# Performance work log

Measured on AMD Instinct MI355X. Metric: run time of the kernel, lower is better.

## Reference

```python
import jax, jax.numpy as jnp
import numpy as np

B, C, H, W = 8, 64, 64, 64
OUT_H, OUT_W = 32, 32


def setup_inputs() -> dict:
    key = jax.random.key(0)
    ks = jax.random.split(key, 9)
    s = 1.0 / np.sqrt(C).astype(np.float32)
    return {
        "x": jax.random.normal(ks[0], (B, C, H, W), jnp.float32),
        "wq": jax.random.normal(ks[1], (C, C), jnp.float32) * s,
        "bq": jax.random.normal(ks[2], (C,), jnp.float32) * 0.01,
        "wk": jax.random.normal(ks[3], (C, C), jnp.float32) * s,
        "bk": jax.random.normal(ks[4], (C,), jnp.float32) * 0.01,
        "wv": jax.random.normal(ks[5], (C, C), jnp.float32) * s,
        "bv": jax.random.normal(ks[6], (C,), jnp.float32) * 0.01,
        "wm": jax.random.normal(ks[7], (C, C), jnp.float32) * s,
        "bm": jax.random.normal(ks[8], (C,), jnp.float32) * 0.01,
    }


def reference(x, wq, bq, wk, bk, wv, bv, wm, bm):
    # pushforward: self-attention over spatial tokens, 1x1-conv mixing + ReLU,
    # then bilinear resize to out_shape (align_corners=False semantics).
    b, c, h, w = x.shape
    t = x.reshape(b, c, h * w).transpose(0, 2, 1)  # [B, HW, C] tokens
    q = jnp.einsum('bnc,dc->bnd', t, wq) + bq      # 1x1 conv == per-pixel linear
    k = jnp.einsum('bnc,dc->bnd', t, wk) + bk
    v = jnp.einsum('bnc,dc->bnd', t, wv) + bv
    scores = jnp.einsum('bnc,bmc->bnm', q, k) / jnp.sqrt(jnp.float32(c))  # [B, HW, HW]
    attn = jax.nn.softmax(scores, axis=-1)
    o = jnp.einsum('bnm,bmc->bnc', attn, v)        # [B, HW, C]
    mixed = jax.nn.relu(jnp.einsum('bnc,dc->bnd', o, wm) + bm)
    out = mixed.transpose(0, 2, 1).reshape(b, c, h, w)
    # F.interpolate(mode='bilinear', align_corners=False) == half-pixel bilinear, no antialias
    out = jax.image.resize(out, (b, c, OUT_H, OUT_W), method='bilinear', antialias=False)
    return out
```

## Files before the change

### kernel.cpp

```cpp
#include <hip/hip_runtime.h>
#include <stdint.h>

typedef unsigned short u16;
typedef unsigned int   u32;
typedef __attribute__((ext_vector_type(8)))  short short8;
typedef __attribute__((ext_vector_type(4)))  float f32x4;
typedef __attribute__((ext_vector_type(16))) float f32x16;

#define NTOK 4096
#define LOG2E 1.44269504088896340736f
#define QS    (0.125f * LOG2E)

__device__ __forceinline__ u16 f2bf(float f) {
    u32 u = __builtin_bit_cast(u32, f);
    u += 0x7fffu + ((u >> 16) & 1u);
    return (u16)(u >> 16);
}
__device__ __forceinline__ float bf2f(u16 v) {
    return __builtin_bit_cast(float, (u32)v << 16);
}
__device__ __forceinline__ u32 pk_hu(float a, float b) {
    u32 ua = __builtin_bit_cast(u32, a) + 0x8000u;
    u32 ub = __builtin_bit_cast(u32, b) + 0x8000u;
    return __builtin_amdgcn_perm(ub, ua, 0x07060302);
}
__device__ __forceinline__ f32x16 zero16() {
    f32x16 v;
#pragma unroll
    for (int i = 0; i < 16; ++i) v[i] = 0.f;
    return v;
}

#define MFMA16x32 __builtin_amdgcn_mfma_f32_16x16x32_bf16
#define MFMA32x16 __builtin_amdgcn_mfma_f32_32x32x16_bf16

__global__ __launch_bounds__(512, 2) void qkv2(
    const float* __restrict__ x,
    const float* __restrict__ wq, const float* __restrict__ bq,
    const float* __restrict__ wk, const float* __restrict__ bk,
    const float* __restrict__ wv, const float* __restrict__ bv,
    u16* __restrict__ Q, u16* __restrict__ K, u16* __restrict__ Vp)
{
    __shared__ __align__(16) u16 Wl[3 * 64 * 72];
    __shared__ __align__(16) u16 Xl[128 * 64];
    const int tid  = threadIdx.x;
    const int b    = blockIdx.x & 7;
    const int sp   = blockIdx.x >> 3;
    const int n0   = sp << 7;
    const int wave = tid >> 6;
    const int lane = tid & 63;
    const int quad = lane >> 4;
    const int l15  = lane & 15;

#pragma unroll
    for (int j = 0; j < 6; ++j) {
        const int idx  = j * 2048 + tid * 4;
        const int mat  = idx >> 12;
        const int ridx = idx & 4095;
        const float* src = (mat == 0) ? wq : (mat == 1) ? wk : wv;
        const float sc = (mat == 0) ? QS : 1.0f;
        const float4 v = *(const float4*)(src + ridx);
        uint2 pk;
        pk.x = (u32)f2bf(v.x * sc) | ((u32)f2bf(v.y * sc) << 16);
        pk.y = (u32)f2bf(v.z * sc) | ((u32)f2bf(v.w * sc) << 16);
        *(uint2*)&Wl[mat * 4608 + (ridx >> 6) * 72 + (ridx & 63)] = pk;
    }

    const int ch = tid >> 3;
    const int tg = tid & 7;
    float4 xs[4];
#pragma unroll
    for (int k = 0; k < 4; ++k)
        xs[k] = *(const float4*)(x + ((size_t)(b * 64 + ch)) * NTOK + n0 + tg * 16 + k * 4);
#pragma unroll
    for (int k = 0; k < 4; ++k) {
        const float vv[4] = {xs[k].x, xs[k].y, xs[k].z, xs[k].w};
#pragma unroll
        for (int e = 0; e < 4; ++e) {
            const int tok = tg * 16 + k * 4 + e;
            Xl[tok * 64 + (((ch >> 3) ^ (tok & 7)) & 7) * 8 + (ch & 7)] = f2bf(vv[e]);
        }
    }
    __syncthreads();

    const int row0 = wave * 16 + l15;
    short8 xf[2];
#pragma unroll
    for (int kk = 0; kk < 2; ++kk)
        xf[kk] = *(const short8*)&Xl[row0 * 64 + (((kk * 4 + quad) ^ (row0 & 7)) & 7) * 8];

    const size_t tokbase = (size_t)b * NTOK + n0 + wave * 16;

#pragma unroll
    for (int mat = 0; mat < 2; ++mat) {
        const float* bias = (mat == 0) ? bq : bk;
        const float bsc = (mat == 0) ? QS : 1.0f;
#pragma unroll
        for (int mt = 0; mt < 4; ++mt) {
            const u16* wr = &Wl[mat * 4608 + (mt * 16 + l15) * 72 + quad * 8];
            const short8 wf0 = *(const short8*)(wr);
            const short8 wf1 = *(const short8*)(wr + 32);
            f32x4 acc = {0.f, 0.f, 0.f, 0.f};
            acc = MFMA16x32(wf0, xf[0], acc, 0, 0, 0);
            acc = MFMA16x32(wf1, xf[1], acc, 0, 0, 0);
            const float4 b4 = *(const float4*)(bias + mt * 16 + quad * 4);
            uint2 pk;
            pk.x = (u32)f2bf(acc[0] + b4.x * bsc) | ((u32)f2bf(acc[1] + b4.y * bsc) << 16);
            pk.y = (u32)f2bf(acc[2] + b4.z * bsc) | ((u32)f2bf(acc[3] + b4.w * bsc) << 16);
            u16* dst = (mat == 0) ? Q : K;
            *(uint2*)(dst + (tokbase + l15) * 64 + mt * 16 + quad * 4) = pk;
        }
    }

    __syncthreads();
    u16* Vl = Xl;
    const int tok = wave * 16 + l15;
    const int th  = tok >> 6;
    const int t64 = tok & 63;
#pragma unroll
    for (int mt = 0; mt < 4; ++mt) {
        const u16* wr = &Wl[2 * 4608 + (mt * 16 + l15) * 72 + quad * 8];
        const short8 wf0 = *(const short8*)(wr);
        const short8 wf1 = *(const short8*)(wr + 32);
        f32x4 acc = {0.f, 0.f, 0.f, 0.f};
        acc = MFMA16x32(wf0, xf[0], acc, 0, 0, 0);
        acc = MFMA16x32(wf1, xf[1], acc, 0, 0, 0);
        const float4 b4 = *(const float4*)(bv + mt * 16 + quad * 4);
        const float o[4] = {acc[0] + b4.x, acc[1] + b4.y, acc[2] + b4.z, acc[3] + b4.w};
#pragma unroll
        for (int r = 0; r < 4; ++r) {
            const int d = mt * 16 + quad * 4 + r;
            Vl[(d * 2 + th) * 64 + (((t64 >> 3) ^ ((d >> 1) & 7)) & 7) * 8 + (t64 & 7)] = f2bf(o[r]);
        }
    }
    __syncthreads();

#pragma unroll
    for (int dd = 0; dd < 4; ++dd) {
        const int id   = dd * 512 + tid;
        const int d2   = id >> 5;
        const int tokc = (id & 31) * 4;
        const int thc  = tokc >> 6;
        const int t64c = tokc & 63;
        const int slot = ((t64c >> 3) ^ ((d2 >> 1) & 7)) & 7;
        const uint2 v2 = *(const uint2*)&Vl[(d2 * 2 + thc) * 64 + slot * 8 + (t64c & 7)];
        const int gt = sp * 4 + (tokc >> 5);
        const int tl = tokc & 31;
        const int sl = (tl & 0x13) | (((tl >> 2) & 1) << 3) | (((tl >> 3) & 1) << 2);
        *(uint2*)(Vp + (((size_t)b * 128 + gt) * 64 + d2) * 32 + sl) = v2;
    }
}

__global__ __launch_bounds__(512, 2) void attn8(
    const u16* __restrict__ Q, const u16* __restrict__ K,
    const u16* __restrict__ Vp,
    const float* __restrict__ wm, const float* __restrict__ bm,
    float* __restrict__ out)
{
    __shared__ __align__(16) char smem[54272];
    const int tid  = threadIdx.x;
    const int wave = tid >> 6;
    const int lane = tid & 63;
    const int c31  = lane & 31;
    const int hw   = lane >> 5;
    const int quad = lane >> 4;
    const int l15  = lane & 15;
    const int h    = wave >> 2;
    const int s    = wave & 3;
    const int b    = blockIdx.x & 7;
    const int oh   = blockIdx.x >> 3;
    const int n0   = oh * 128;

    short8 qf[2][4];
#pragma unroll
    for (int nt = 0; nt < 2; ++nt)
#pragma unroll
        for (int ks = 0; ks < 4; ++ks)
            qf[nt][ks] = *(const short8*)(Q + ((size_t)(b * NTOK + n0 + h * 64 + nt * 32 + c31)) * 64
                                            + ks * 16 + hw * 8);

    const u16* Kb  = K + ((size_t)b * NTOK + s * 1024) * 64;
    const u16* Vbp = Vp + ((size_t)b * 128 + s * 32) * 2048;

    f32x16 O[2][2];
#pragma unroll
    for (int mt = 0; mt < 2; ++mt)
#pragma unroll
        for (int nt = 0; nt < 2; ++nt) O[mt][nt] = zero16();
    float lpa[2] = {0.f, 0.f};

    auto load_kv = [&](short8 (&kf)[4], short8 (&vf)[4], int t) {
        const int tc = (t < 32) ? t : 31;
        const u16* kt = Kb + (size_t)tc * 2048;
#pragma unroll
        for (int ks = 0; ks < 4; ++ks)
            kf[ks] = *(const short8*)(kt + c31 * 64 + ks * 16 + hw * 8);
        const u16* vt = Vbp + (size_t)tc * 2048;
#pragma unroll
        for (int mk = 0; mk < 4; ++mk)
            vf[mk] = *(const short8*)(vt + ((mk >> 1) * 32 + c31) * 32 + (mk & 1) * 16 + hw * 8);
    };

    auto S_compute = [&](f32x16 (&sv)[2], const short8 (&kf)[4]) {
#pragma unroll
        for (int nt = 0; nt < 2; ++nt) {
            f32x16 a = zero16();
            a = MFMA32x16(kf[0], qf[nt][0], a, 0, 0, 0);
            a = MFMA32x16(kf[1], qf[nt][1], a, 0, 0, 0);
            a = MFMA32x16(kf[2], qf[nt][2], a, 0, 0, 0);
            a = MFMA32x16(kf[3], qf[nt][3], a, 0, 0, 0);
            sv[nt] = a;
        }
    };

    auto tile_tail = [&](const f32x16 (&sv)[2], const short8 (&vf)[4]) {
#pragma unroll
        for (int nt = 0; nt < 2; ++nt) {
            float p[16];
#pragma unroll
            for (int r = 0; r < 16; ++r) p[r] = __builtin_amdgcn_exp2f(sv[nt][r]);
            lpa[nt] += (((p[0] + p[1]) + (p[2] + p[3])) + ((p[4] + p[5]) + (p[6] + p[7])))
                     + (((p[8] + p[9]) + (p[10] + p[11])) + ((p[12] + p[13]) + (p[14] + p[15])));
            uint4 B0, B1;
            B0.x = pk_hu(p[0],  p[1]);  B0.y = pk_hu(p[2],  p[3]);
            B0.z = pk_hu(p[4],  p[5]);  B0.w = pk_hu(p[6],  p[7]);
            B1.x = pk_hu(p[8],  p[9]);  B1.y = pk_hu(p[10], p[11]);
            B1.z = pk_hu(p[12], p[13]); B1.w = pk_hu(p[14], p[15]);
            const short8 pb0 = __builtin_bit_cast(short8, B0);
            const short8 pb1 = __builtin_bit_cast(short8, B1);
            O[0][nt] = MFMA32x16(vf[0], pb0, O[0][nt], 0, 0, 0);
            O[0][nt] = MFMA32x16(vf[1], pb1, O[0][nt], 0, 0, 0);
            O[1][nt] = MFMA32x16(vf[2], pb0, O[1][nt], 0, 0, 0);
            O[1][nt] = MFMA32x16(vf[3], pb1, O[1][nt], 0, 0, 0);
        }
    };

    short8 kfA[4], vfA[4], kfB[4], vfB[4];
    f32x16 svA[2], svB[2];
    load_kv(kfA, vfA, 0);
    load_kv(kfB, vfB, 1);
    S_compute(svA, kfA);

#pragma unroll 1
    for (int tt = 0; tt < 16; ++tt) {
        const int t0 = tt * 2;
        S_compute(svB, kfB);
        tile_tail(svA, vfA);
        load_kv(kfA, vfA, t0 + 2);
        S_compute(svA, kfA);
        tile_tail(svB, vfB);
        load_kv(kfB, vfB, t0 + 3);
    }

#pragma unroll
    for (int nt = 0; nt < 2; ++nt) lpa[nt] += __shfl_xor(lpa[nt], 32);

    float* lpbuf = (float*)(smem + 52224);
    if (hw == 0) {
#pragma unroll
        for (int nt = 0; nt < 2; ++nt)
            lpbuf[(h * 4 + s) * 64 + nt * 32 + c31] = lpa[nt];
    }
    if (s != 0) {
        u16* sec = (u16*)smem + (h * 3 + s - 1) * 4352;
#pragma unroll
        for (int mt = 0; mt < 2; ++mt)
#pragma unroll
            for (int nt = 0; nt < 2; ++nt)
#pragma unroll
                for (int r = 0; r < 16; ++r) {
                    const int ch = mt * 32 + (r & 3) + 8 * (r >> 2) + 4 * hw;
                    sec[(nt * 32 + c31) * 68 + ch] = f2bf(O[mt][nt][r]);
                }
    }
    __syncthreads();

    float rinv[2];
    if (s == 0) {
#pragma unroll
        for (int nt = 0; nt < 2; ++nt) {
            float sum = 0.f;
#pragma unroll
            for (int sx = 0; sx < 4; ++sx)
                sum += lpbuf[(h * 4 + sx) * 64 + nt * 32 + c31];
            rinv[nt] = 1.0f / sum;
        }
#pragma unroll
        for (int sx = 1; sx < 4; ++sx) {
            const u16* sec = (const u16*)smem + (h * 3 + sx - 1) * 4352;
#pragma unroll
            for (int mt = 0; mt < 2; ++mt)
#pragma unroll
                for (int nt = 0; nt < 2; ++nt)
#pragma unroll
                    for (int r = 0; r < 16; ++r) {
                        const int ch = mt * 32 + (r & 3) + 8 * (r >> 2) + 4 * hw;
                        O[mt][nt][r] += bf2f(sec[(nt * 32 + c31) * 68 + ch]);
                    }
        }
    }
    short8 wB[4][2];
    float bb[4];
#pragma unroll
    for (int nt = 0; nt < 4; ++nt) {
        const int d = nt * 16 + l15;
        const float* wr = wm + (size_t)d * 64 + quad * 8;
        const float4 a0 = *(const float4*)(wr);
        const float4 a1 = *(const float4*)(wr + 4);
        const float4 c0 = *(const float4*)(wr + 32);
        const float4 c1 = *(const float4*)(wr + 36);
        ((u32*)&wB[nt][0])[0] = (u32)f2bf(a0.x) | ((u32)f2bf(a0.y) << 16);
        ((u32*)&wB[nt][0])[1] = (u32)f2bf(a0.z) | ((u32)f2bf(a0.w) << 16);
        ((u32*)&wB[nt][0])[2] = (u32)f2bf(a1.x) | ((u32)f2bf(a1.y) << 16);
        ((u32*)&wB[nt][0])[3] = (u32)f2bf(a1.z) | ((u32)f2bf(a1.w) << 16);
        ((u32*)&wB[nt][1])[0] = (u32)f2bf(c0.x) | ((u32)f2bf(c0.y) << 16);
        ((u32*)&wB[nt][1])[1] = (u32)f2bf(c0.z) | ((u32)f2bf(c0.w) << 16);
        ((u32*)&wB[nt][1])[2] = (u32)f2bf(c1.x) | ((u32)f2bf(c1.y) << 16);
        ((u32*)&wB[nt][1])[3] = (u32)f2bf(c1.z) | ((u32)f2bf(c1.w) << 16);
        bb[nt] = bm[d];
    }
    __syncthreads();

    if (s == 0) {
        u16* M0 = (u16*)smem + h * 4096;
#pragma unroll
        for (int mt = 0; mt < 2; ++mt)
#pragma unroll
            for (int nt = 0; nt < 2; ++nt)
#pragma unroll
                for (int r = 0; r < 16; ++r) {
                    const int lr = nt * 32 + c31;
                    const int ch = mt * 32 + (r & 3) + 8 * (r >> 2) + 4 * hw;
                    const float v = O[mt][nt][r] * rinv[nt];
                    M0[lr * 64 + (((ch >> 3) ^ (lr & 7)) & 7) * 8 + (ch & 7)] = f2bf(v);
                }
    }
    __syncthreads();

    const u16* M0r = (const u16*)smem + (wave >> 2) * 4096;
    const int lr = (wave & 3) * 16 + l15;
    const short8 af0 = *(const short8*)&M0r[lr * 64 + ((quad ^ (lr & 7)) & 7) * 8];
    const short8 af1 = *(const short8*)&M0r[lr * 64 + (((4 + quad) ^ (lr & 7)) & 7) * 8];
    float* Mf = (float*)(smem + 16384);
#pragma unroll
    for (int nt = 0; nt < 4; ++nt) {
        f32x4 acc = {0.f, 0.f, 0.f, 0.f};
        acc = MFMA16x32(af0, wB[nt][0], acc, 0, 0, 0);
        acc = MFMA16x32(af1, wB[nt][1], acc, 0, 0, 0);
#pragma unroll
        for (int r = 0; r < 4; ++r) {
            float v = acc[r] + bb[nt];
            v = v > 0.f ? v : 0.f;
            Mf[(wave * 16 + quad * 4 + r) * 68 + nt * 16 + l15] = v;
        }
    }
    __syncthreads();

    const int ow = tid & 31;
    const int cb = (tid >> 5) & 15;
#pragma unroll
    for (int i = 0; i < 4; ++i) {
        const int c = cb + i * 16;
        const float v = 0.25f * (Mf[(2 * ow) * 68 + c] + Mf[(2 * ow + 1) * 68 + c]
                               + Mf[(64 + 2 * ow) * 68 + c] + Mf[(65 + 2 * ow) * 68 + c]);
        out[((size_t)(b * 64 + c) * 32 + oh) * 32 + ow] = v;
    }
}

extern "C" void kernel_launch(void* const* d_in, const int* in_sizes, int n_in,
                              void* d_out, int out_size, void* d_ws, size_t ws_size,
                              hipStream_t stream) {
    (void)in_sizes; (void)n_in; (void)out_size; (void)ws_size;
    const float* x  = (const float*)d_in[0];
    const float* wq = (const float*)d_in[1];
    const float* bq = (const float*)d_in[2];
    const float* wk = (const float*)d_in[3];
    const float* bk = (const float*)d_in[4];
    const float* wv = (const float*)d_in[5];
    const float* bv = (const float*)d_in[6];
    const float* wm = (const float*)d_in[7];
    const float* bm = (const float*)d_in[8];

    u16* Q  = (u16*)d_ws;
    u16* K  = Q + (size_t)8 * NTOK * 64;
    u16* Vp = K + (size_t)8 * NTOK * 64;

    qkv2<<<256, 512, 0, stream>>>(x, wq, bq, wk, bk, wv, bv, Q, K, Vp);
    attn8<<<256, 512, 0, stream>>>(Q, K, Vp, wm, bm, (float*)d_out);
}
```

Baseline: 136.0 us.

## Fuse QKV projection and attention into one kernel with grid-wide barrier

```diff
diff --git a/kernel.cpp b/kernel.cpp
--- a/kernel.cpp
+++ b/kernel.cpp
@@ -34,15 +34,16 @@
 #define MFMA16x32 __builtin_amdgcn_mfma_f32_16x16x32_bf16
 #define MFMA32x16 __builtin_amdgcn_mfma_f32_32x32x16_bf16
 
-__global__ __launch_bounds__(512, 2) void qkv2(
+__global__ __launch_bounds__(512, 2) void fused_qkv_attn(
     const float* __restrict__ x,
     const float* __restrict__ wq, const float* __restrict__ bq,
     const float* __restrict__ wk, const float* __restrict__ bk,
     const float* __restrict__ wv, const float* __restrict__ bv,
-    u16* __restrict__ Q, u16* __restrict__ K, u16* __restrict__ Vp)
+    const float* __restrict__ wm, const float* __restrict__ bm,
+    u16* __restrict__ K, u16* __restrict__ Vp, u32* __restrict__ ctr,
+    float* __restrict__ out)
 {
-    __shared__ __align__(16) u16 Wl[3 * 64 * 72];
-    __shared__ __align__(16) u16 Xl[128 * 64];
+    __shared__ __align__(16) char smem[62464];
     const int tid  = threadIdx.x;
     const int b    = blockIdx.x & 7;
     const int sp   = blockIdx.x >> 3;
@@ -51,6 +52,10 @@
     const int lane = tid & 63;
     const int quad = lane >> 4;
     const int l15  = lane & 15;
+
+    u16* Wl   = (u16*)smem;
+    u16* Xl   = (u16*)(smem + 27648);
+    u16* Qlds = (u16*)(smem + 44032);
 
 #pragma unroll
     for (int j = 0; j < 6; ++j) {
@@ -66,118 +71,127 @@
         *(uint2*)&Wl[mat * 4608 + (ridx >> 6) * 72 + (ridx & 63)] = pk;
     }
 
-    const int ch = tid >> 3;
-    const int tg = tid & 7;
-    float4 xs[4];
-#pragma unroll
-    for (int k = 0; k < 4; ++k)
-        xs[k] = *(const float4*)(x + ((size_t)(b * 64 + ch)) * NTOK + n0 + tg * 16 + k * 4);
-#pragma unroll
-    for (int k = 0; k < 4; ++k) {
-        const float vv[4] = {xs[k].x, xs[k].y, xs[k].z, xs[k].w};
-#pragma unroll
-        for (int e = 0; e < 4; ++e) {
-            const int tok = tg * 16 + k * 4 + e;
-            Xl[tok * 64 + (((ch >> 3) ^ (tok & 7)) & 7) * 8 + (ch & 7)] = f2bf(vv[e]);
-        }
-    }
-    __syncthreads();
-
-    const int row0 = wave * 16 + l15;
-    short8 xf[2];
-#pragma unroll
-    for (int kk = 0; kk < 2; ++kk)
-        xf[kk] = *(const short8*)&Xl[row0 * 64 + (((kk * 4 + quad) ^ (row0 & 7)) & 7) * 8];
-
-    const size_t tokbase = (size_t)b * NTOK + n0 + wave * 16;
-
-#pragma unroll
-    for (int mat = 0; mat < 2; ++mat) {
-        const float* bias = (mat == 0) ? bq : bk;
-        const float bsc = (mat == 0) ? QS : 1.0f;
+    {
+        const int ch = tid >> 3;
+        const int tg = tid & 7;
+        float4 xs[4];
+#pragma unroll
+        for (int k = 0; k < 4; ++k)
+            xs[k] = *(const float4*)(x + ((size_t)(b * 64 + ch)) * NTOK + n0 + tg * 16 + k * 4);
+#pragma unroll
+        for (int k = 0; k < 4; ++k) {
+            const float vv[4] = {xs[k].x, xs[k].y, xs[k].z, xs[k].w};
+#pragma unroll
+            for (int e = 0; e < 4; ++e) {
+                const int tok = tg * 16 + k * 4 + e;
+                Xl[tok * 64 + (((ch >> 3) ^ (tok & 7)) & 7) * 8 + (ch & 7)] = f2bf(vv[e]);
+            }
+        }
+    }
+    __syncthreads();
+
+    {
+        const int row0 = wave * 16 + l15;
+        short8 xf[2];
+#pragma unroll
+        for (int kk = 0; kk < 2; ++kk)
+            xf[kk] = *(const short8*)&Xl[row0 * 64 + (((kk * 4 + quad) ^ (row0 & 7)) & 7) * 8];
+
+#pragma unroll
+        for (int mat = 0; mat < 2; ++mat) {
+            const float* bias = (mat == 0) ? bq : bk;
+            const float bsc = (mat == 0) ? QS : 1.0f;
+#pragma unroll
+            for (int mt = 0; mt < 4; ++mt) {
+                const u16* wr = &Wl[mat * 4608 + (mt * 16 + l15) * 72 + quad * 8];
+                const short8 wf0 = *(const short8*)(wr);
+                const short8 wf1 = *(const short8*)(wr + 32);
+                f32x4 acc = {0.f, 0.f, 0.f, 0.f};
+                acc = MFMA16x32(wf0, xf[0], acc, 0, 0, 0);
+                acc = MFMA16x32(wf1, xf[1], acc, 0, 0, 0);
+                const float4 b4 = *(const float4*)(bias + mt * 16 + quad * 4);
+                const float o[4] = {acc[0] + b4.x * bsc, acc[1] + b4.y * bsc,
+                                    acc[2] + b4.z * bsc, acc[3] + b4.w * bsc};
+                if (mat == 0) {
+                    const int tok = wave * 16 + l15;
+#pragma unroll
+                    for (int r = 0; r < 4; ++r) {
+                        const int d = mt * 16 + quad * 4 + r;
+                        Qlds[tok * 64 + (((d >> 3) ^ (tok & 7)) & 7) * 8 + (d & 7)] = f2bf(o[r]);
+                    }
+                } else {
+                    uint2 pk;
+                    pk.x = (u32)f2bf(o[0]) | ((u32)f2bf(o[1]) << 16);
+                    pk.y = (u32)f2bf(o[2]) | ((u32)f2bf(o[3]) << 16);
+                    *(uint2*)(K + ((size_t)(b * NTOK + n0 + wave * 16 + l15)) * 64
+                                + mt * 16 + quad * 4) = pk;
+                }
+            }
+        }
+
+        __syncthreads();
+        u16* Vl = Xl;
+        const int tok = wave * 16 + l15;
+        const int th  = tok >> 6;
+        const int t64 = tok & 63;
 #pragma unroll
         for (int mt = 0; mt < 4; ++mt) {
-            const u16* wr = &Wl[mat * 4608 + (mt * 16 + l15) * 72 + quad * 8];
+            const u16* wr = &Wl[2 * 4608 + (mt * 16 + l15) * 72 + quad * 8];
             const short8 wf0 = *(const short8*)(wr);
             const short8 wf1 = *(const short8*)(wr + 32);
             f32x4 acc = {0.f, 0.f, 0.f, 0.f};
             acc = MFMA16x32(wf0, xf[0], acc, 0, 0, 0);
             acc = MFMA16x32(wf1, xf[1], acc, 0, 0, 0);
-            const float4 b4 = *(const float4*)(bias + mt * 16 + quad * 4);
-            uint2 pk;
-            pk.x = (u32)f2bf(acc[0] + b4.x * bsc) | ((u32)f2bf(acc[1] + b4.y * bsc) << 16);
-            pk.y = (u32)f2bf(acc[2] + b4.z * bsc) | ((u32)f2bf(acc[3] + b4.w * bsc) << 16);
-            u16* dst = (mat == 0) ? Q : K;
-            *(uint2*)(dst + (tokbase + l15) * 64 + mt * 16 + quad * 4) = pk;
-        }
-    }
-
-    __syncthreads();
-    u16* Vl = Xl;
-    const int tok = wave * 16 + l15;
-    const int th  = tok >> 6;
-    const int t64 = tok & 63;
-#pragma unroll
-    for (int mt = 0; mt < 4; ++mt) {
-        const u16* wr = &Wl[2 * 4608 + (mt * 16 + l15) * 72 + quad * 8];
-        const short8 wf0 = *(const short8*)(wr);
-        const short8 wf1 = *(const short8*)(wr + 32);
-        f32x4 acc = {0.f, 0.f, 0.f, 0.f};
-        acc = MFMA16x32(wf0, xf[0], acc, 0, 0, 0);
-        acc = MFMA16x32(wf1, xf[1], acc, 0, 0, 0);
-        const float4 b4 = *(const float4*)(bv + mt * 16 + quad * 4);
-        const float o[4] = {acc[0] + b4.x, acc[1] + b4.y, acc[2] + b4.z, acc[3] + b4.w};
-#pragma unroll
-        for (int r = 0; r < 4; ++r) {
-            const int d = mt * 16 + quad * 4 + r;
-            Vl[(d * 2 + th) * 64 + (((t64 >> 3) ^ ((d >> 1) & 7)) & 7) * 8 + (t64 & 7)] = f2bf(o[r]);
-        }
-    }
-    __syncthreads();
-
-#pragma unroll
-    for (int dd = 0; dd < 4; ++dd) {
-        const int id   = dd * 512 + tid;
-        const int d2   = id >> 5;
-        const int tokc = (id & 31) * 4;
-        const int thc  = tokc >> 6;
-        const int t64c = tokc & 63;
-        const int slot = ((t64c >> 3) ^ ((d2 >> 1) & 7)) & 7;
-        const uint2 v2 = *(const uint2*)&Vl[(d2 * 2 + thc) * 64 + slot * 8 + (t64c & 7)];
-        const int gt = sp * 4 + (tokc >> 5);
-        const int tl = tokc & 31;
-        const int sl = (tl & 0x13) | (((tl >> 2) & 1) << 3) | (((tl >> 3) & 1) << 2);
-        *(uint2*)(Vp + (((size_t)b * 128 + gt) * 64 + d2) * 32 + sl) = v2;
-    }
-}
-
-__global__ __launch_bounds__(512, 2) void attn8(
-    const u16* __restrict__ Q, const u16* __restrict__ K,
-    const u16* __restrict__ Vp,
-    const float* __restrict__ wm, const float* __restrict__ bm,
-    float* __restrict__ out)
-{
-    __shared__ __align__(16) char smem[54272];
-    const int tid  = threadIdx.x;
-    const int wave = tid >> 6;
-    const int lane = tid & 63;
-    const int c31  = lane & 31;
-    const int hw   = lane >> 5;
-    const int quad = lane >> 4;
-    const int l15  = lane & 15;
-    const int h    = wave >> 2;
-    const int s    = wave & 3;
-    const int b    = blockIdx.x & 7;
-    const int oh   = blockIdx.x >> 3;
-    const int n0   = oh * 128;
+            const float4 b4 = *(const float4*)(bv + mt * 16 + quad * 4);
+            const float o[4] = {acc[0] + b4.x, acc[1] + b4.y, acc[2] + b4.z, acc[3] + b4.w};
+#pragma unroll
+            for (int r = 0; r < 4; ++r) {
+                const int d = mt * 16 + quad * 4 + r;
+                Vl[(d * 2 + th) * 64 + (((t64 >> 3) ^ ((d >> 1) & 7)) & 7) * 8 + (t64 & 7)] = f2bf(o[r]);
+            }
+        }
+        __syncthreads();
+
+#pragma unroll
+        for (int dd = 0; dd < 4; ++dd) {
+            const int id   = dd * 512 + tid;
+            const int d2   = id >> 5;
+            const int tokc = (id & 31) * 4;
+            const int thc  = tokc >> 6;
+            const int t64c = tokc & 63;
+            const int slot = ((t64c >> 3) ^ ((d2 >> 1) & 7)) & 7;
+            const uint2 v2 = *(const uint2*)&Vl[(d2 * 2 + thc) * 64 + slot * 8 + (t64c & 7)];
+            const int gt = sp * 4 + (tokc >> 5);
+            const int tl = tokc & 31;
+            const int sl = (tl & 0x13) | (((tl >> 2) & 1) << 3) | (((tl >> 3) & 1) << 2);
+            *(uint2*)(Vp + (((size_t)b * 128 + gt) * 64 + d2) * 32 + sl) = v2;
+        }
+    }
+
+    __threadfence();
+    __syncthreads();
+    if (tid == 0) {
+        __hip_atomic_fetch_add(ctr, 1u, __ATOMIC_RELEASE, __HIP_MEMORY_SCOPE_AGENT);
+        while (__hip_atomic_load(ctr, __ATOMIC_ACQUIRE, __HIP_MEMORY_SCOPE_AGENT) < 256u)
+            __builtin_amdgcn_s_sleep(8);
+    }
+    __syncthreads();
+    __threadfence();
+
+    const int c31 = lane & 31;
+    const int hw  = lane >> 5;
+    const int h   = wave >> 2;
+    const int s   = wave & 3;
 
     short8 qf[2][4];
 #pragma unroll
     for (int nt = 0; nt < 2; ++nt)
 #pragma unroll
-        for (int ks = 0; ks < 4; ++ks)
-            qf[nt][ks] = *(const short8*)(Q + ((size_t)(b * NTOK + n0 + h * 64 + nt * 32 + c31)) * 64
-                                            + ks * 16 + hw * 8);
+        for (int ks = 0; ks < 4; ++ks) {
+            const int tok = h * 64 + nt * 32 + c31;
+            const int slot = ((ks * 2 + hw) ^ (tok & 7)) & 7;
+            qf[nt][ks] = *(const short8*)&Qlds[tok * 64 + slot * 8];
+        }
 
     const u16* Kb  = K + ((size_t)b * NTOK + s * 1024) * 64;
     const u16* Vbp = Vp + ((size_t)b * 128 + s * 32) * 2048;
@@ -200,7 +214,6 @@
         for (int mk = 0; mk < 4; ++mk)
             vf[mk] = *(const short8*)(vt + ((mk >> 1) * 32 + c31) * 32 + (mk & 1) * 16 + hw * 8);
     };
-
     auto S_compute = [&](f32x16 (&sv)[2], const short8 (&kf)[4]) {
 #pragma unroll
         for (int nt = 0; nt < 2; ++nt) {
@@ -212,7 +225,6 @@
             sv[nt] = a;
         }
     };
-
     auto tile_tail = [&](const f32x16 (&sv)[2], const short8 (&vf)[4]) {
 #pragma unroll
         for (int nt = 0; nt < 2; ++nt) {
@@ -363,7 +375,7 @@
         const int c = cb + i * 16;
         const float v = 0.25f * (Mf[(2 * ow) * 68 + c] + Mf[(2 * ow + 1) * 68 + c]
                                + Mf[(64 + 2 * ow) * 68 + c] + Mf[(65 + 2 * ow) * 68 + c]);
-        out[((size_t)(b * 64 + c) * 32 + oh) * 32 + ow] = v;
+        out[((size_t)(b * 64 + c) * 32 + sp) * 32 + ow] = v;
     }
 }
 
@@ -381,10 +393,11 @@
     const float* wm = (const float*)d_in[7];
     const float* bm = (const float*)d_in[8];
 
-    u16* Q  = (u16*)d_ws;
-    u16* K  = Q + (size_t)8 * NTOK * 64;
+    u16* K  = (u16*)d_ws;
     u16* Vp = K + (size_t)8 * NTOK * 64;
-
-    qkv2<<<256, 512, 0, stream>>>(x, wq, bq, wk, bk, wv, bv, Q, K, Vp);
-    attn8<<<256, 512, 0, stream>>>(Q, K, Vp, wm, bm, (float*)d_out);
-}
+    u32* ctr = (u32*)((char*)d_ws + (size_t)16 * 1024 * 1024 / 2);
+
+    hipMemsetAsync(ctr, 0, 64, stream);
+    fused_qkv_attn<<<256, 512, 0, stream>>>(x, wq, bq, wk, bk, wv, bv, wm, bm,
+                                            K, Vp, ctr, (float*)d_out);
+}
```

Measured after the change: 213.9 us. +57.3%, slower.
